# Optimization experiments

Measured on AMD Instinct MI355X. Metric: run time of the kernel, lower is better.

Reference implementation:

```python
import jax, jax.numpy as jnp
import numpy as np

B, T, D, H, L, W = 32, 512, 256, 8, 2, 10
NQ = 10000
HD = D // H


def setup_inputs():
    key = jax.random.key(0)
    ks = jax.random.split(key, 16)
    def n(k, shape, s=0.02):
        return jax.random.normal(k, shape, jnp.float32) * s
    return {
        "q": jax.random.randint(ks[0], (B, T), 0, NQ),
        "s": jax.random.randint(ks[1], (B, T), 0, 2),
        "q_embed": n(ks[2], (NQ + 1, D)),
        "s_embed": n(ks[3], (2, D)),
        "pos_embed": n(ks[4], (512, D)),
        "fusion_w": n(ks[5], (2 * D, D)),
        "fusion_b": jnp.zeros((D,), jnp.float32),
        "in_proj_w": n(ks[6], (L, D, 3 * D)),
        "in_proj_b": jnp.zeros((L, 3 * D), jnp.float32),
        "out_proj_w": n(ks[7], (L, D, D)),
        "out_proj_b": jnp.zeros((L, D), jnp.float32),
        "ln1_g": jnp.ones((L, D), jnp.float32),
        "ln1_b": jnp.zeros((L, D), jnp.float32),
        "ln2_g": jnp.ones((L, D), jnp.float32),
        "ln2_b": jnp.zeros((L, D), jnp.float32),
        "ff1_w": n(ks[8], (L, D, 4 * D)),
        "ff1_b": jnp.zeros((L, 4 * D), jnp.float32),
        "ff2_w": n(ks[9], (L, 4 * D, D)),
        "ff2_b": jnp.zeros((L, D), jnp.float32),
        "sw1": n(ks[10], (6, 32), 0.1),
        "sb1": jnp.zeros((32,), jnp.float32),
        "sw2": n(ks[11], (32, D // 4), 0.1),
        "sb2": jnp.zeros((D // 4,), jnp.float32),
        "cw1": n(ks[12], (D + D // 4, D)),
        "cb1": jnp.zeros((D,), jnp.float32),
        "cw2": n(ks[13], (D, 1)),
        "cb2": jnp.zeros((1,), jnp.float32),
    }


def _ln(x, g, b):
    mu = jnp.mean(x, -1, keepdims=True)
    var = jnp.mean(jnp.square(x - mu), -1, keepdims=True)
    return (x - mu) * jax.lax.rsqrt(var + 1e-5) * g + b


def _sliding_sum(x, w):
    # sum over trailing window of size w ending at each t, via prefix sums
    c = jnp.concatenate([jnp.zeros((x.shape[0], 1), x.dtype), jnp.cumsum(x, axis=1)], axis=1)
    t = jnp.arange(x.shape[1])
    return c[:, t + 1] - c[:, jnp.maximum(t + 1 - w, 0)]


def _stats(s, mask):
    # vectorized version of _extract_statistics (prefix-sum sliding windows)
    mf = mask.astype(jnp.float32)
    sf = s.astype(jnp.float32) * mf
    valid = _sliding_sum(mf, W)
    correct_rate = _sliding_sum(sf, W) / (valid + 1e-6)
    rc = _sliding_sum(mf, 5)
    recent_correct = _sliding_sum(sf, 5) / (rc + 1e-6)
    trans = ((s[:, 1:] != s[:, :-1]) & mask[:, 1:] & mask[:, :-1]).astype(jnp.float32)
    diff = jnp.concatenate([jnp.zeros((s.shape[0], 1), jnp.float32), trans], axis=1)
    change_rate = _sliding_sum(diff, W - 1) / (valid + 1e-6)
    # max consecutive equal run within each trailing window of size W
    sp = jnp.pad(s, ((0, 0), (W - 1, 0)))
    mp = jnp.pad(mask, ((0, 0), (W - 1, 0)))
    win_s = [sp[:, j:j + T] for j in range(W)]
    win_m = [mp[:, j:j + T] for j in range(W)]
    run = win_m[0].astype(jnp.float32)
    mx = run
    for j in range(1, W):  # fixed small window, not a data-dim loop
        eq = (win_s[j] == win_s[j - 1]) & win_m[j - 1]
        run = win_m[j].astype(jnp.float32) * (jnp.where(eq, run, 0.0) + 1.0)
        mx = jnp.maximum(mx, run)
    rel = jnp.broadcast_to(jnp.arange(T, dtype=jnp.float32) / max(T, 100), s.shape)
    cov = valid / W
    return jnp.stack([correct_rate, recent_correct, change_rate, mx / W, rel, cov], axis=-1)


def reference(q, s, q_embed, s_embed, pos_embed, fusion_w, fusion_b, in_proj_w, in_proj_b,
              out_proj_w, out_proj_b, ln1_g, ln1_b, ln2_g, ln2_b, ff1_w, ff1_b, ff2_w, ff2_b,
              sw1, sb1, sw2, sb2, cw1, cb1, cw2, cb2):
    mask = s >= 0
    qm = jnp.where(mask, q, 0)
    sm = jnp.where(mask, s, 0)
    h = jnp.concatenate([q_embed[qm], s_embed[sm]], axis=-1)  # [B,T,2D]
    h = jax.nn.relu(h @ fusion_w + fusion_b) + pos_embed[:T][None]
    causal = jnp.tril(jnp.ones((T, T), bool))
    allowed = causal[None, None] & mask[:, None, None, :]
    scale = 1.0 / (HD ** 0.5)
    for l in range(L):
        qkv = h @ in_proj_w[l] + in_proj_b[l]
        qh, kh, vh = jnp.split(qkv, 3, axis=-1)
        qh = qh.reshape(B, T, H, HD).transpose(0, 2, 1, 3)
        kh = kh.reshape(B, T, H, HD).transpose(0, 2, 1, 3)
        vh = vh.reshape(B, T, H, HD).transpose(0, 2, 1, 3)
        scores = jnp.einsum('bhqd,bhkd->bhqk', qh, kh) * scale
        scores = jnp.where(allowed, scores, -1e9)
        attn = jax.nn.softmax(scores, axis=-1)
        o = jnp.einsum('bhqk,bhkd->bhqd', attn, vh).transpose(0, 2, 1, 3).reshape(B, T, D)
        h = _ln(h + (o @ out_proj_w[l] + out_proj_b[l]), ln1_g[l], ln1_b[l])
        ff = jax.nn.gelu(h @ ff1_w[l] + ff1_b[l], approximate=False) @ ff2_w[l] + ff2_b[l]
        h = _ln(h + ff, ln2_g[l], ln2_b[l])
    sfeat = _stats(sm, mask)  # [B,T,6]
    semb = jax.nn.relu(sfeat @ sw1 + sb1) @ sw2 + sb2  # [B,T,D//4]
    comb = jnp.concatenate([h, semb], axis=-1)
    logits = (jax.nn.relu(comb @ cw1 + cb1) @ cw2 + cb2)[..., 0]
    return jnp.where(mask, logits, -1e9)
```

## Files before the change

kernel.cpp:

```cpp
#include <hip/hip_runtime.h>
#include <hip/hip_bf16.h>
#include <cmath>


using short8 = __attribute__((ext_vector_type(8))) short;
using short4v = __attribute__((ext_vector_type(4))) short;
using f32x4  = __attribute__((ext_vector_type(4))) float;

__device__ inline float gelu_f(float x) {
    return 0.5f * x * (1.0f + erff(x * 0.70710678118654752f));
}

__device__ inline short f2bf(float x) {
    union { float f; unsigned u; } v; v.f = x;
    return (short)((v.u + 0x7fffu + ((v.u >> 16) & 1u)) >> 16);
}

__device__ inline float bf2f(short v) {
    union { unsigned u; float f; } x; x.u = ((unsigned)(unsigned short)v) << 16;
    return x.f;
}

__device__ inline unsigned packbf(float lo, float hi) {
    union { float f; unsigned u; } a, b; a.f = lo; b.f = hi;
    unsigned ra = (a.u + 0x7fffu + ((a.u >> 16) & 1u)) >> 16;
    unsigned rb = (b.u + 0x7fffu + ((b.u >> 16) & 1u)) >> 16;
    return (rb << 16) | (ra & 0xffffu);
}

#define GLOAD16(gp, lp) __builtin_amdgcn_global_load_lds( \
    (const __attribute__((address_space(1))) void*)(gp), \
    (__attribute__((address_space(3))) void*)(lp), 16, 0, 0)

#define WAITVM(n) asm volatile("s_waitcnt vmcnt(" #n ")" ::: "memory")

__global__ __launch_bounds__(256) void prep_kernel(
    const float* __restrict__ fusion_w, const float* __restrict__ in_proj_w,
    const float* __restrict__ out_proj_w, const float* __restrict__ ff1_w,
    const float* __restrict__ ff2_w, const float* __restrict__ cw1,
    short* __restrict__ wts,
    const int* __restrict__ q, const int* __restrict__ s,
    const float* __restrict__ qe, const float* __restrict__ se,
    short* __restrict__ A)
{
    __shared__ float tile[32][33];
    if (blockIdx.x < 1744) {
        const int b0[10]      = {0,128,320,512,576,640,896,1152,1408,1664};
        const int Ks[10]      = {512,256,256,256,256,256,256,1024,1024,320};
        const int Ns[10]      = {256,768,768,256,256,1024,1024,256,256,256};
        const int sidx[10]    = {0,1,1,2,2,3,3,4,4,5};
        const size_t soff[10] = {0,0,196608,0,65536,0,262144,0,262144,0};
        const size_t doff[10] = {0,131072,327680,524288,589824,655360,917504,1179648,1441792,1703936};
        const float* srcs[6] = {fusion_w, in_proj_w, out_proj_w, ff1_w, ff2_w, cw1};
        int bid = blockIdx.x;
        int mi = 0;
        while (mi < 9 && bid >= b0[mi + 1]) ++mi;
        int bl = bid - b0[mi];
        int K = Ks[mi], N = Ns[mi];
        int tx = bl % (N >> 5), ty = bl / (N >> 5);
        const float* src = srcs[sidx[mi]] + soff[mi];
        short* dst = wts + doff[mi];
        int c = threadIdx.x & 31, r = threadIdx.x >> 5;
#pragma unroll
        for (int i = 0; i < 4; ++i)
            tile[r + i * 8][c] = src[(size_t)(ty * 32 + r + i * 8) * N + tx * 32 + c];
        __syncthreads();
#pragma unroll
        for (int i = 0; i < 4; ++i)
            dst[(size_t)(tx * 32 + r + i * 8) * K + ty * 32 + c] = f2bf(tile[c][r + i * 8]);
    } else {
        int e8 = (blockIdx.x - 1744) * 256 + threadIdx.x;
        int row = e8 >> 6;
        int k8 = (e8 & 63) << 3;
        int sv = s[row];
        bool mk = sv >= 0;
        const float* src = (k8 < 256) ? qe + (size_t)(mk ? q[row] : 0) * 256 + k8
                                      : se + (size_t)(mk ? sv : 0) * 256 + (k8 - 256);
        float4 v0 = *(const float4*)src;
        float4 v1 = *(const float4*)(src + 4);
        short8 o;
        o[0] = f2bf(v0.x); o[1] = f2bf(v0.y); o[2] = f2bf(v0.z); o[3] = f2bf(v0.w);
        o[4] = f2bf(v1.x); o[5] = f2bf(v1.y); o[6] = f2bf(v1.z); o[7] = f2bf(v1.w);
        *(short8*)(A + (size_t)row * 512 + k8) = o;
    }
}

template<int EPI, int BM, int BN, int PANELS>
__global__ __launch_bounds__(256, (BM == 128) ? 3 : 2) void gemm_pipe(
    const short* __restrict__ A, const short* __restrict__ A2,
    const short* __restrict__ Wt, const float* __restrict__ bias,
    short* __restrict__ hb, short* __restrict__ oq, short* __restrict__ ok,
    short* __restrict__ ov,
    const float* __restrict__ gamma, const float* __restrict__ beta,
    const float* __restrict__ pos, const float* __restrict__ cw2,
    const float* __restrict__ cb2, const int* __restrict__ smask,
    float* __restrict__ outlog, int N, int K)
{
    constexpr int WC = BN / 64;
    constexpr int L = BM / 64 + BN / 64;
    const int tid = threadIdx.x, lane = tid & 63, wv = tid >> 6;
    const int lg = lane >> 4, lr = lane & 15;
    const int wr = wv / WC, wc = wv % WC;
    const int bid = blockIdx.x;
    const int p = (bid >> 3) % PANELS;
    const int y = ((bid >> 3) / PANELS) * 8 + (bid & 7);
    const int m0 = y * BM, n0 = p * BN;

    __shared__ short As[3][BM * 32];
    __shared__ short Bs[3][BN * 32];
    __shared__ float redS[64][4];
    __shared__ float redQ[64][4];

    f32x4 acc[4][4] = {};
    const int nsteps = K >> 5;

    auto stage = [&](int buf, int step) {
        int k0 = step << 5;
#pragma unroll
        for (int i = 0; i < BM / 64; ++i) {
            int slot = i * 256 + tid;
            int g = slot / BM, m = slot % BM;
            int k = k0 + g * 8;
            const short* src;
            if constexpr (EPI == 4)
                src = (k < 256) ? A + (size_t)(m0 + m) * 256 + k
                                : A2 + (size_t)(m0 + m) * 64 + (k - 256);
            else
                src = A + (size_t)(m0 + m) * K + k;
            GLOAD16(src, &As[buf][slot * 8]);
        }
#pragma unroll
        for (int i = 0; i < BN / 64; ++i) {
            int slot = i * 256 + tid;
            int g = slot / BN, n = slot % BN;
            GLOAD16(Wt + (size_t)(n0 + n) * K + k0 + g * 8, &Bs[buf][slot * 8]);
        }
    };

    stage(0, 0);
    stage(1, 1);
    int cur = 0;
    for (int t = 0; t < nsteps; ++t) {
        if (t + 2 < nsteps) {
            int c2 = cur + 2; if (c2 >= 3) c2 -= 3;
            stage(c2, t + 2);
            if constexpr (L == 4) WAITVM(8); else WAITVM(10);
        } else if (t + 1 < nsteps) {
            if constexpr (L == 4) WAITVM(4); else WAITVM(5);
        } else {
            WAITVM(0);
        }
        __builtin_amdgcn_s_barrier();
        __builtin_amdgcn_sched_barrier(0);
        short8 a[4], b[4];
#pragma unroll
        for (int i = 0; i < 4; ++i)
            a[i] = *(const short8*)&As[cur][(lg * BM + wr * 64 + i * 16 + lr) * 8];
#pragma unroll
        for (int j = 0; j < 4; ++j)
            b[j] = *(const short8*)&Bs[cur][(lg * BN + wc * 64 + j * 16 + lr) * 8];
#pragma unroll
        for (int i = 0; i < 4; ++i)
#pragma unroll
            for (int j = 0; j < 4; ++j)
                acc[i][j] = __builtin_amdgcn_mfma_f32_16x16x32_bf16(a[i], b[j], acc[i][j], 0, 0, 0);
        __builtin_amdgcn_sched_barrier(0);
        __builtin_amdgcn_s_barrier();
        cur = (cur == 2) ? 0 : cur + 1;
    }

    if constexpr (EPI == 0) {
#pragma unroll
        for (int i = 0; i < 4; ++i)
#pragma unroll
        for (int j = 0; j < 4; ++j)
#pragma unroll
        for (int r = 0; r < 4; ++r) {
            int row = m0 + wr * 64 + i * 16 + lg * 4 + r;
            int col = n0 + wc * 64 + j * 16 + lr;
            float x = acc[i][j][r] + bias[col];
            x = fmaxf(x, 0.f) + pos[(size_t)(row & 511) * 256 + col];
            hb[(size_t)row * 256 + col] = f2bf(x);
        }
    } else if constexpr (EPI == 1) {
#pragma unroll
        for (int i = 0; i < 4; ++i)
#pragma unroll
        for (int j = 0; j < 4; ++j)
#pragma unroll
        for (int r = 0; r < 4; ++r) {
            int row = m0 + wr * 64 + i * 16 + lg * 4 + r;
            int gcol = n0 + wc * 64 + j * 16 + lr;
            int t = row & 511, bg = row >> 9;
            int sec = gcol >> 8, cc = gcol & 255;
            int h = cc >> 5, d = cc & 31, bh = bg * 8 + h;
            short v = f2bf(acc[i][j][r] + bias[gcol]);
            if (sec == 0)      oq[((size_t)bh * 512 + t) * 32 + d] = v;
            else if (sec == 1) ok[((size_t)bh * 512 + t) * 32 + d] = v;
            else {
                int kl = t & 31;
                ov[(size_t)bh * 16384 + (size_t)(t >> 5) * 1024 +
                   (size_t)((kl >> 2) & 3) * 256 + d * 8 + (((kl & 3) << 1) | ((kl >> 4) & 1))] = v;
            }
        }
    } else if constexpr (EPI == 2) {
#pragma unroll
        for (int i = 0; i < 4; ++i)
#pragma unroll
        for (int j = 0; j < 4; ++j)
#pragma unroll
        for (int r = 0; r < 4; ++r) {
            int row = m0 + wr * 64 + i * 16 + lg * 4 + r;
            int gcol = n0 + wc * 64 + j * 16 + lr;
            float x = acc[i][j][r] + bias[gcol];
            oq[(size_t)row * N + gcol] = f2bf(gelu_f(x));
        }
    } else if constexpr (EPI == 3) {
        float ps[4][4], pq[4][4];
#pragma unroll
        for (int i = 0; i < 4; ++i)
#pragma unroll
        for (int r = 0; r < 4; ++r) { ps[i][r] = 0.f; pq[i][r] = 0.f; }
#pragma unroll
        for (int i = 0; i < 4; ++i)
#pragma unroll
        for (int j = 0; j < 4; ++j)
#pragma unroll
        for (int r = 0; r < 4; ++r) {
            int row = m0 + i * 16 + lg * 4 + r;
            int col = wc * 64 + j * 16 + lr;
            float x = acc[i][j][r] + bias[col] + bf2f(hb[(size_t)row * 256 + col]);
            acc[i][j][r] = x;
            ps[i][r] += x; pq[i][r] += x * x;
        }
#pragma unroll
        for (int off = 1; off < 16; off <<= 1)
#pragma unroll
            for (int i = 0; i < 4; ++i)
#pragma unroll
            for (int r = 0; r < 4; ++r) {
                ps[i][r] += __shfl_xor(ps[i][r], off);
                pq[i][r] += __shfl_xor(pq[i][r], off);
            }
        if (lr == 0) {
#pragma unroll
            for (int i = 0; i < 4; ++i)
#pragma unroll
            for (int r = 0; r < 4; ++r) {
                int rl = i * 16 + lg * 4 + r;
                redS[rl][wc] = ps[i][r]; redQ[rl][wc] = pq[i][r];
            }
        }
        __syncthreads();
#pragma unroll
        for (int i = 0; i < 4; ++i)
#pragma unroll
        for (int r = 0; r < 4; ++r) {
            int rl = i * 16 + lg * 4 + r;
            int row = m0 + rl;
            float sm = redS[rl][0] + redS[rl][1] + redS[rl][2] + redS[rl][3];
            float sq = redQ[rl][0] + redQ[rl][1] + redQ[rl][2] + redQ[rl][3];
            float mu = sm * (1.f / 256.f);
            float var = sq * (1.f / 256.f) - mu * mu;
            float rstd = rsqrtf(var + 1e-5f);
#pragma unroll
            for (int j = 0; j < 4; ++j) {
                int col = wc * 64 + j * 16 + lr;
                float yv = (acc[i][j][r] - mu) * rstd * gamma[col] + beta[col];
                hb[(size_t)row * 256 + col] = f2bf(yv);
            }
        }
    } else {
        float pa[4][4];
#pragma unroll
        for (int i = 0; i < 4; ++i)
#pragma unroll
        for (int r = 0; r < 4; ++r) pa[i][r] = 0.f;
#pragma unroll
        for (int i = 0; i < 4; ++i)
#pragma unroll
        for (int j = 0; j < 4; ++j)
#pragma unroll
        for (int r = 0; r < 4; ++r) {
            int col = wc * 64 + j * 16 + lr;
            float x = fmaxf(acc[i][j][r] + bias[col], 0.f);
            pa[i][r] += x * cw2[col];
        }
#pragma unroll
        for (int off = 1; off < 16; off <<= 1)
#pragma unroll
            for (int i = 0; i < 4; ++i)
#pragma unroll
            for (int r = 0; r < 4; ++r) pa[i][r] += __shfl_xor(pa[i][r], off);
        if (lr == 0) {
#pragma unroll
            for (int i = 0; i < 4; ++i)
#pragma unroll
            for (int r = 0; r < 4; ++r)
                redS[i * 16 + lg * 4 + r][wc] = pa[i][r];
        }
        __syncthreads();
        if (tid < 64) {
            int row = m0 + tid;
            float v = redS[tid][0] + redS[tid][1] + redS[tid][2] + redS[tid][3] + cb2[0];
            outlog[row] = (smask[row] >= 0) ? v : -1e9f;
        }
    }
}

__global__ __launch_bounds__(256) void attn_mfma(
    const short* __restrict__ Qg, const short* __restrict__ Kg,
    const short* __restrict__ VTg, short* __restrict__ O)
{
    __shared__ unsigned Wp[4][16][20];
    const int bh = blockIdx.x >> 2, part = blockIdx.x & 3;
    const int b = bh >> 3, h = bh & 7;
    const int wv = threadIdx.x >> 6, lane = threadIdx.x & 63;
    const int lg = lane >> 4, lr = lane & 15;
    const int slot = part * 4 + wv;
    const short* Qbh = Qg + (size_t)bh * 16384;
    const short* Kbh = Kg + (size_t)bh * 16384;
    const short* Vbh = VTg + (size_t)bh * 16384;
    const float scale = 0.17677669529663687f;

    for (int half = 0; half < 2; ++half) {
        const int tile = half ? (31 - slot) : slot;
        const int q0 = tile << 4;
        short8 qa = *(const short8*)(Qbh + (size_t)(q0 + lr) * 32 + lg * 8);
        f32x4 o0 = {}, o1 = {};
        float l_[4] = {0.f, 0.f, 0.f, 0.f};
        const int nfull = q0 >> 5;

        for (int c = 0; c <= nfull; ++c) {
            int kc = c << 5;
            short8 kf0 = *(const short8*)(Kbh + (size_t)(kc + lr) * 32 + lg * 8);
            short8 kf1 = *(const short8*)(Kbh + (size_t)(kc + 16 + lr) * 32 + lg * 8);
            f32x4 s0 = {}, s1 = {};
            s0 = __builtin_amdgcn_mfma_f32_16x16x32_bf16(qa, kf0, s0, 0, 0, 0);
            s1 = __builtin_amdgcn_mfma_f32_16x16x32_bf16(qa, kf1, s1, 0, 0, 0);
            float p0[4], p1[4];
            if (c < nfull) {
#pragma unroll
                for (int r = 0; r < 4; ++r) {
                    p0[r] = __expf(s0[r] * scale);
                    p1[r] = __expf(s1[r] * scale);
                }
            } else {
#pragma unroll
                for (int r = 0; r < 4; ++r) {
                    int qq = q0 + lg * 4 + r;
                    p0[r] = (kc + lr)      > qq ? 0.f : __expf(s0[r] * scale);
                    p1[r] = (kc + 16 + lr) > qq ? 0.f : __expf(s1[r] * scale);
                }
            }
#pragma unroll
            for (int r = 0; r < 4; ++r) {
                l_[r] += p0[r] + p1[r];
                Wp[wv][lg * 4 + r][lr] = packbf(p0[r], p1[r]);
            }
            short8 pa = *(const short8*)&Wp[wv][lr][lg * 4];
            short8 vf0 = *(const short8*)(Vbh + (size_t)c * 1024 + lg * 256 + lr * 8);
            short8 vf1 = *(const short8*)(Vbh + (size_t)c * 1024 + lg * 256 + (lr + 16) * 8);
            o0 = __builtin_amdgcn_mfma_f32_16x16x32_bf16(pa, vf0, o0, 0, 0, 0);
            o1 = __builtin_amdgcn_mfma_f32_16x16x32_bf16(pa, vf1, o1, 0, 0, 0);
        }
#pragma unroll
        for (int off = 1; off < 16; off <<= 1)
#pragma unroll
            for (int r = 0; r < 4; ++r) l_[r] += __shfl_xor(l_[r], off);
#pragma unroll
        for (int r = 0; r < 4; ++r) {
            float inv = 1.f / l_[r];
            size_t ro = ((size_t)b * 512 + q0 + lg * 4 + r) * 256 + h * 32;
            O[ro + lr] = f2bf(o0[r] * inv);
            O[ro + 16 + lr] = f2bf(o1[r] * inv);
        }
    }
}

__global__ __launch_bounds__(512) void stats_kernel(
    const int* __restrict__ s, short* __restrict__ semb,
    const float* __restrict__ sw1, const float* __restrict__ sb1,
    const float* __restrict__ sw2, const float* __restrict__ sb2)
{
    __shared__ float sv_sh[512];
    __shared__ float m_sh[512];
    __shared__ float sw2_sh[2048];
    const int b = blockIdx.x;
    const int t = threadIdx.x;
    {
        int sval = s[b * 512 + t];
        bool mk = sval >= 0;
        sv_sh[t] = mk ? (float)sval : 0.f;
        m_sh[t] = mk ? 1.f : 0.f;
    }
    for (int i = t; i < 2048; i += 512) sw2_sh[i] = sw2[i];
    __syncthreads();

    float mf10 = 0, sf10 = 0, mf5 = 0, sf5 = 0, d9 = 0;
#pragma unroll
    for (int k = 0; k < 10; ++k) {
        int idx = t - k;
        if (idx >= 0) {
            float mv = m_sh[idx], sv = sv_sh[idx];
            mf10 += mv; sf10 += sv;
            if (k < 5) { mf5 += mv; sf5 += sv; }
            if (k < 9 && idx >= 1) {
                if (sv != sv_sh[idx - 1] && mv > 0.5f && m_sh[idx - 1] > 0.5f) d9 += 1.f;
            }
        }
    }
    float run, mx;
    {
        int x0 = t - 9;
        run = (x0 >= 0) ? m_sh[x0] : 0.f;
        mx = run;
#pragma unroll
        for (int j = 1; j < 10; ++j) {
            int xc = t + j - 9, xp = xc - 1;
            float sc = (xc >= 0) ? sv_sh[xc] : 0.f;
            float sp = (xp >= 0) ? sv_sh[xp] : 0.f;
            float mc = (xc >= 0) ? m_sh[xc] : 0.f;
            float mp = (xp >= 0) ? m_sh[xp] : 0.f;
            bool eq = (sc == sp) && (mp > 0.5f);
            run = (mc > 0.5f) ? ((eq ? run : 0.f) + 1.f) : 0.f;
            mx = fmaxf(mx, run);
        }
    }
    float f[6];
    f[0] = sf10 / (mf10 + 1e-6f);
    f[1] = sf5 / (mf5 + 1e-6f);
    f[2] = d9 / (mf10 + 1e-6f);
    f[3] = mx * 0.1f;
    f[4] = (float)t * (1.f / 512.f);
    f[5] = mf10 * 0.1f;

    float hid[32];
#pragma unroll
    for (int j2 = 0; j2 < 32; ++j2) {
        float a = sb1[j2];
#pragma unroll
        for (int i = 0; i < 6; ++i) a = fmaf(f[i], sw1[i * 32 + j2], a);
        hid[j2] = fmaxf(a, 0.f);
    }
    short* orow = semb + ((size_t)b * 512 + t) * 64;
    for (int c = 0; c < 64; c += 4) {
        float v0 = sb2[c], v1 = sb2[c + 1], v2 = sb2[c + 2], v3 = sb2[c + 3];
#pragma unroll
        for (int j2 = 0; j2 < 32; ++j2) {
            float hh = hid[j2];
            v0 = fmaf(hh, sw2_sh[j2 * 64 + c], v0);
            v1 = fmaf(hh, sw2_sh[j2 * 64 + c + 1], v1);
            v2 = fmaf(hh, sw2_sh[j2 * 64 + c + 2], v2);
            v3 = fmaf(hh, sw2_sh[j2 * 64 + c + 3], v3);
        }
        short4v o; o[0] = f2bf(v0); o[1] = f2bf(v1); o[2] = f2bf(v2); o[3] = f2bf(v3);
        *(short4v*)(orow + c) = o;
    }
}

extern "C" void kernel_launch(void* const* d_in, const int* in_sizes, int n_in,
                              void* d_out, int out_size, void* d_ws, size_t ws_size,
                              hipStream_t stream) {
    const int*   q         = (const int*)d_in[0];
    const int*   s         = (const int*)d_in[1];
    const float* q_embed   = (const float*)d_in[2];
    const float* s_embed   = (const float*)d_in[3];
    const float* pos_embed = (const float*)d_in[4];
    const float* fusion_w  = (const float*)d_in[5];
    const float* fusion_b  = (const float*)d_in[6];
    const float* in_proj_w = (const float*)d_in[7];
    const float* in_proj_b = (const float*)d_in[8];
    const float* out_proj_w= (const float*)d_in[9];
    const float* out_proj_b= (const float*)d_in[10];
    const float* ln1_g     = (const float*)d_in[11];
    const float* ln1_b     = (const float*)d_in[12];
    const float* ln2_g     = (const float*)d_in[13];
    const float* ln2_b     = (const float*)d_in[14];
    const float* ff1_w     = (const float*)d_in[15];
    const float* ff1_b     = (const float*)d_in[16];
    const float* ff2_w     = (const float*)d_in[17];
    const float* ff2_b     = (const float*)d_in[18];
    const float* sw1       = (const float*)d_in[19];
    const float* sb1       = (const float*)d_in[20];
    const float* sw2       = (const float*)d_in[21];
    const float* sb2       = (const float*)d_in[22];
    const float* cw1       = (const float*)d_in[23];
    const float* cb1       = (const float*)d_in[24];
    const float* cw2       = (const float*)d_in[25];
    const float* cb2       = (const float*)d_in[26];
    float* out = (float*)d_out;

    char* base = (char*)d_ws;
    short* hb   = (short*)(base);
    short* bufA = (short*)(base + 8388608);
    short* att  = (short*)(base + 41943040);
    short* Qg   = (short*)(base + 50331648);
    short* Kg   = (short*)(base + 58720256);
    short* VTg  = (short*)(base + 67108864);
    short* semb = (short*)(base + 75497472);
    short* wts  = (short*)(base + 77594624);

    const size_t W_FUSION = 0, W_INPROJ0 = 131072, W_INPROJ1 = 327680;
    const size_t W_OUTPROJ0 = 524288, W_OUTPROJ1 = 589824;
    const size_t W_FF1_0 = 655360, W_FF1_1 = 917504;
    const size_t W_FF2_0 = 1179648, W_FF2_1 = 1441792;
    const size_t W_CW1 = 1703936;

    prep_kernel<<<5840, 256, 0, stream>>>(fusion_w, in_proj_w, out_proj_w,
                                          ff1_w, ff2_w, cw1, wts,
                                          q, s, q_embed, s_embed, bufA);
    gemm_pipe<0, 128, 128, 2><<<256, 256, 0, stream>>>(bufA, nullptr,
        wts + W_FUSION, fusion_b, hb, nullptr, nullptr, nullptr,
        nullptr, nullptr, pos_embed, nullptr, nullptr, nullptr, nullptr, 256, 512);
    for (int l = 0; l < 2; ++l) {
        gemm_pipe<1, 128, 128, 6><<<768, 256, 0, stream>>>(hb, nullptr,
            wts + (l ? W_INPROJ1 : W_INPROJ0), in_proj_b + l * 768,
            nullptr, Qg, Kg, VTg, nullptr, nullptr, nullptr, nullptr, nullptr,
            nullptr, nullptr, 768, 256);
        attn_mfma<<<1024, 256, 0, stream>>>(Qg, Kg, VTg, att);
        gemm_pipe<3, 64, 256, 1><<<256, 256, 0, stream>>>(att, nullptr,
            wts + (l ? W_OUTPROJ1 : W_OUTPROJ0), out_proj_b + l * 256,
            hb, nullptr, nullptr, nullptr, ln1_g + l * 256, ln1_b + l * 256,
            nullptr, nullptr, nullptr, nullptr, nullptr, 256, 256);
        gemm_pipe<2, 128, 128, 8><<<1024, 256, 0, stream>>>(hb, nullptr,
            wts + (l ? W_FF1_1 : W_FF1_0), ff1_b + l * 1024,
            nullptr, bufA, nullptr, nullptr, nullptr, nullptr, nullptr,
            nullptr, nullptr, nullptr, nullptr, 1024, 256);
        gemm_pipe<3, 64, 256, 1><<<256, 256, 0, stream>>>(bufA, nullptr,
            wts + (l ? W_FF2_1 : W_FF2_0), ff2_b + l * 256,
            hb, nullptr, nullptr, nullptr, ln2_g + l * 256, ln2_b + l * 256,
            nullptr, nullptr, nullptr, nullptr, nullptr, 256, 1024);
    }
    stats_kernel<<<32, 512, 0, stream>>>(s, semb, sw1, sb1, sw2, sb2);
    gemm_pipe<4, 64, 256, 1><<<256, 256, 0, stream>>>(hb, semb,
        wts + W_CW1, cb1, nullptr, nullptr, nullptr, nullptr, nullptr, nullptr,
        nullptr, cw2, cb2, s, out, 256, 320);
}
```

Baseline: 335.4 us.

## Add stationary-weight GEMM kernel for fusion, QKV and FF1 projections

```diff
diff --git a/kernel.cpp b/kernel.cpp
--- a/kernel.cpp
+++ b/kernel.cpp
@@ -85,16 +85,98 @@
     }
 }
 
+template<int EPI, int BN, int K>
+__global__ __launch_bounds__(512) void gemm_bstat(
+    const short* __restrict__ A, const short* __restrict__ Wt,
+    const float* __restrict__ bias, short* __restrict__ out0,
+    short* __restrict__ ok, short* __restrict__ ov,
+    const float* __restrict__ pos)
+{
+    constexpr int SPR = K / 8;
+    constexpr int NSTEP = K / 32;
+    constexpr int NJ = BN / 16;
+    __shared__ short Bs[BN * K];
+    const int tid = threadIdx.x, lane = tid & 63, wv = tid >> 6;
+    const int lg = lane >> 4, lr = lane & 15;
+    const int n0 = blockIdx.y * BN;
+    const int row0 = blockIdx.x * 128 + wv * 16;
+
+#pragma unroll
+    for (int i = 0; i < (BN * K) / 4096; ++i) {
+        int slot = i * 512 + tid;
+        int n = slot / SPR, posn = slot % SPR;
+        int g = posn ^ (n & 7);
+        GLOAD16(Wt + (size_t)(n0 + n) * K + g * 8, &Bs[slot * 8]);
+    }
+    const short* arow = A + (size_t)(row0 + lr) * K;
+    short8 af[NSTEP];
+#pragma unroll
+    for (int kk = 0; kk < NSTEP; ++kk)
+        af[kk] = *(const short8*)(arow + kk * 32 + lg * 8);
+    __syncthreads();
+
+    f32x4 acc[NJ] = {};
+#pragma unroll
+    for (int kk = 0; kk < NSTEP; ++kk) {
+#pragma unroll
+        for (int j = 0; j < NJ; ++j) {
+            int n = j * 16 + lr;
+            short8 b = *(const short8*)&Bs[n * K + (((kk * 4 + lg) ^ (n & 7)) << 3)];
+            acc[j] = __builtin_amdgcn_mfma_f32_16x16x32_bf16(af[kk], b, acc[j], 0, 0, 0);
+        }
+    }
+
+    if constexpr (EPI == 0) {
+#pragma unroll
+        for (int j = 0; j < NJ; ++j)
+#pragma unroll
+        for (int r = 0; r < 4; ++r) {
+            int row = row0 + lg * 4 + r;
+            int col = n0 + j * 16 + lr;
+            float x = acc[j][r] + bias[col];
+            x = fmaxf(x, 0.f) + pos[(size_t)(row & 511) * 256 + col];
+            out0[(size_t)row * 256 + col] = f2bf(x);
+        }
+    } else if constexpr (EPI == 1) {
+#pragma unroll
+        for (int j = 0; j < NJ; ++j)
+#pragma unroll
+        for (int r = 0; r < 4; ++r) {
+            int row = row0 + lg * 4 + r;
+            int gcol = n0 + j * 16 + lr;
+            int t = row & 511, bg = row >> 9;
+            int sec = gcol >> 8, cc = gcol & 255;
+            int h = cc >> 5, d = cc & 31, bh = bg * 8 + h;
+            short v = f2bf(acc[j][r] + bias[gcol]);
+            if (sec == 0)      out0[((size_t)bh * 512 + t) * 32 + d] = v;
+            else if (sec == 1) ok[((size_t)bh * 512 + t) * 32 + d] = v;
+            else {
+                int kl = t & 31;
+                ov[(size_t)bh * 16384 + (size_t)(t >> 5) * 1024 +
+                   (size_t)((kl >> 2) & 3) * 256 + d * 8 + (((kl & 3) << 1) | ((kl >> 4) & 1))] = v;
+            }
+        }
+    } else {
+#pragma unroll
+        for (int j = 0; j < NJ; ++j)
+#pragma unroll
+        for (int r = 0; r < 4; ++r) {
+            int row = row0 + lg * 4 + r;
+            int gcol = n0 + j * 16 + lr;
+            float x = acc[j][r] + bias[gcol];
+            out0[(size_t)row * 1024 + gcol] = f2bf(gelu_f(x));
+        }
+    }
+}
+
 template<int EPI, int BM, int BN, int PANELS>
-__global__ __launch_bounds__(256, (BM == 128) ? 3 : 2) void gemm_pipe(
+__global__ __launch_bounds__(256) void gemm_pipe(
     const short* __restrict__ A, const short* __restrict__ A2,
     const short* __restrict__ Wt, const float* __restrict__ bias,
-    short* __restrict__ hb, short* __restrict__ oq, short* __restrict__ ok,
-    short* __restrict__ ov,
+    short* __restrict__ hb,
     const float* __restrict__ gamma, const float* __restrict__ beta,
-    const float* __restrict__ pos, const float* __restrict__ cw2,
-    const float* __restrict__ cb2, const int* __restrict__ smask,
-    float* __restrict__ outlog, int N, int K)
+    const float* __restrict__ cw2, const float* __restrict__ cb2,
+    const int* __restrict__ smask, float* __restrict__ outlog, int N, int K)
 {
     constexpr int WC = BN / 64;
     constexpr int L = BM / 64 + BN / 64;
@@ -169,53 +251,7 @@
         cur = (cur == 2) ? 0 : cur + 1;
     }
 
-    if constexpr (EPI == 0) {
-#pragma unroll
-        for (int i = 0; i < 4; ++i)
-#pragma unroll
-        for (int j = 0; j < 4; ++j)
-#pragma unroll
-        for (int r = 0; r < 4; ++r) {
-            int row = m0 + wr * 64 + i * 16 + lg * 4 + r;
-            int col = n0 + wc * 64 + j * 16 + lr;
-            float x = acc[i][j][r] + bias[col];
-            x = fmaxf(x, 0.f) + pos[(size_t)(row & 511) * 256 + col];
-            hb[(size_t)row * 256 + col] = f2bf(x);
-        }
-    } else if constexpr (EPI == 1) {
-#pragma unroll
-        for (int i = 0; i < 4; ++i)
-#pragma unroll
-        for (int j = 0; j < 4; ++j)
-#pragma unroll
-        for (int r = 0; r < 4; ++r) {
-            int row = m0 + wr * 64 + i * 16 + lg * 4 + r;
-            int gcol = n0 + wc * 64 + j * 16 + lr;
-            int t = row & 511, bg = row >> 9;
-            int sec = gcol >> 8, cc = gcol & 255;
-            int h = cc >> 5, d = cc & 31, bh = bg * 8 + h;
-            short v = f2bf(acc[i][j][r] + bias[gcol]);
-            if (sec == 0)      oq[((size_t)bh * 512 + t) * 32 + d] = v;
-            else if (sec == 1) ok[((size_t)bh * 512 + t) * 32 + d] = v;
-            else {
-                int kl = t & 31;
-                ov[(size_t)bh * 16384 + (size_t)(t >> 5) * 1024 +
-                   (size_t)((kl >> 2) & 3) * 256 + d * 8 + (((kl & 3) << 1) | ((kl >> 4) & 1))] = v;
-            }
-        }
-    } else if constexpr (EPI == 2) {
-#pragma unroll
-        for (int i = 0; i < 4; ++i)
-#pragma unroll
-        for (int j = 0; j < 4; ++j)
-#pragma unroll
-        for (int r = 0; r < 4; ++r) {
-            int row = m0 + wr * 64 + i * 16 + lg * 4 + r;
-            int gcol = n0 + wc * 64 + j * 16 + lr;
-            float x = acc[i][j][r] + bias[gcol];
-            oq[(size_t)row * N + gcol] = f2bf(gelu_f(x));
-        }
-    } else if constexpr (EPI == 3) {
+    if constexpr (EPI == 3) {
         float ps[4][4], pq[4][4];
 #pragma unroll
         for (int i = 0; i < 4; ++i)
@@ -510,30 +546,27 @@
     prep_kernel<<<5840, 256, 0, stream>>>(fusion_w, in_proj_w, out_proj_w,
                                           ff1_w, ff2_w, cw1, wts,
                                           q, s, q_embed, s_embed, bufA);
-    gemm_pipe<0, 128, 128, 2><<<256, 256, 0, stream>>>(bufA, nullptr,
-        wts + W_FUSION, fusion_b, hb, nullptr, nullptr, nullptr,
-        nullptr, nullptr, pos_embed, nullptr, nullptr, nullptr, nullptr, 256, 512);
+    gemm_bstat<0, 64, 512><<<dim3(128, 4), 512, 0, stream>>>(bufA,
+        wts + W_FUSION, fusion_b, hb, nullptr, nullptr, pos_embed);
     for (int l = 0; l < 2; ++l) {
-        gemm_pipe<1, 128, 128, 6><<<768, 256, 0, stream>>>(hb, nullptr,
+        gemm_bstat<1, 128, 256><<<dim3(128, 6), 512, 0, stream>>>(hb,
             wts + (l ? W_INPROJ1 : W_INPROJ0), in_proj_b + l * 768,
-            nullptr, Qg, Kg, VTg, nullptr, nullptr, nullptr, nullptr, nullptr,
-            nullptr, nullptr, 768, 256);
+            Qg, Kg, VTg, nullptr);
         attn_mfma<<<1024, 256, 0, stream>>>(Qg, Kg, VTg, att);
         gemm_pipe<3, 64, 256, 1><<<256, 256, 0, stream>>>(att, nullptr,
             wts + (l ? W_OUTPROJ1 : W_OUTPROJ0), out_proj_b + l * 256,
-            hb, nullptr, nullptr, nullptr, ln1_g + l * 256, ln1_b + l * 256,
-            nullptr, nullptr, nullptr, nullptr, nullptr, 256, 256);
-        gemm_pipe<2, 128, 128, 8><<<1024, 256, 0, stream>>>(hb, nullptr,
+            hb, ln1_g + l * 256, ln1_b + l * 256,
+            nullptr, nullptr, nullptr, nullptr, 256, 256);
+        gemm_bstat<2, 128, 256><<<dim3(128, 8), 512, 0, stream>>>(hb,
             wts + (l ? W_FF1_1 : W_FF1_0), ff1_b + l * 1024,
-            nullptr, bufA, nullptr, nullptr, nullptr, nullptr, nullptr,
-            nullptr, nullptr, nullptr, nullptr, 1024, 256);
+            bufA, nullptr, nullptr, nullptr);
         gemm_pipe<3, 64, 256, 1><<<256, 256, 0, stream>>>(bufA, nullptr,
             wts + (l ? W_FF2_1 : W_FF2_0), ff2_b + l * 256,
-            hb, nullptr, nullptr, nullptr, ln2_g + l * 256, ln2_b + l * 256,
-            nullptr, nullptr, nullptr, nullptr, nullptr, 256, 1024);
+            hb, ln2_g + l * 256, ln2_b + l * 256,
+            nullptr, nullptr, nullptr, nullptr, 256, 1024);
     }
     stats_kernel<<<32, 512, 0, stream>>>(s, semb, sw1, sb1, sw2, sb2);
     gemm_pipe<4, 64, 256, 1><<<256, 256, 0, stream>>>(hb, semb,
-        wts + W_CW1, cb1, nullptr, nullptr, nullptr, nullptr, nullptr, nullptr,
-        nullptr, cw2, cb2, s, out, 256, 320);
-}
+        wts + W_CW1, cb1, nullptr, nullptr, nullptr,
+        cw2, cb2, s, out, 256, 320);
+}
```

After: 303.7 us. -9.5%, faster.
